# Kernel optimization log

Hardware: AMD Instinct MI355X
Metric: run time of the kernel (lower is better)

## Reference

```python
import jax, jax.numpy as jnp
import numpy as np

GF_R = 49      # guided filter radius (hardcoded in module)
GF_EPS = 1.0   # guided filter eps (hardcoded in module)


def edge_pad(x, r):
    # replicate-pad last two dims by r
    return jnp.pad(x, ((0, 0), (0, 0), (r, r), (r, r)), mode='edge')


def boxfilter(x, r):
    # integral-image box filter via cumsum chains, same shape out
    p = edge_pad(x, r)
    c = jnp.cumsum(p, axis=3)
    d = c[:, :, :, 2 * r:] - c[:, :, :, :-2 * r]
    c2 = jnp.cumsum(d, axis=2)
    return c2[:, :, 2 * r:, :] - c2[:, :, :-2 * r, :]


def guided_filter(x, r=GF_R, eps=GF_EPS):
    N = boxfilter(jnp.ones_like(x), r)
    mean_x = boxfilter(x, r) / N
    mean_x2 = boxfilter(x * x, r) / N
    var_x = mean_x2 - mean_x * mean_x   # cov_xy == var_x in the original code
    A = var_x / (var_x + eps)
    bb = mean_x - A * mean_x
    A = boxfilter(A, r) / N
    bb = boxfilter(bb, r) / N
    return A * x + bb


def setup_inputs() -> dict:
    key = jax.random.key(0)
    ks = jax.random.split(key, 12)
    m, n, r = 2048, 4096, 4
    m3 = len(np.arange(m)[::3])  # 683
    return {
        'b': jax.random.normal(ks[0], (1, 1, m, n), jnp.float32),
        'b_negative': jax.random.normal(ks[1], (1, 1, m3, n), jnp.float32),
        'foreground_b': jax.random.uniform(ks[2], (1, 1, m, n), jnp.float32),
        'hX': jax.random.normal(ks[3], (1, 1, m * r, n), jnp.float32),
        'recon_old': jax.random.normal(ks[4], (1, 1, m, n), jnp.float32),
        'fusion_mask': jax.random.uniform(ks[5], (1, 1, m, n), jnp.float32),
        'b_old': jax.random.normal(ks[6], (1, 1, m, n), jnp.float32),
        'r': r,
        'w': jax.random.normal(ks[7], (m, n), jnp.float32),
        'decay_col': jax.random.normal(ks[8], (1, 1, m3, n), jnp.float32),
        'ww': jax.random.normal(ks[9], (m, n), jnp.float32),
    }


def reference(b, b_negative, foreground_b, hX, recon_old, fusion_mask, b_old, r, w, decay_col, ww):
    m, n = w.shape
    b = b * jax.nn.softplus(w)
    # cumsum over coarse rows then bilinear upsample to (m, n)
    decay = jnp.cumsum(b_negative * jax.nn.softplus(decay_col), axis=-2)
    decay = jax.image.resize(decay, (1, 1, m, n), method='linear')
    b = jnp.cumsum(b, axis=-2)
    b = b + decay * (1.0 - foreground_b)
    b_adpt = b * fusion_mask + b_old * (1.0 - fusion_mask)
    diff = guided_filter(hX[:, :, ::r, :] + b_adpt - recon_old)
    diff_adpt = jnp.clip(jnp.diff(diff, axis=-2, prepend=diff[:, :, 0:1, :]), 0.0, None)
    diff_adpt = diff_adpt * jax.nn.softplus(ww)
    diff_adpt = jnp.cumsum(diff_adpt, axis=-2)
    b_adpt = b_adpt - diff_adpt
    return (b_adpt, diff, diff_adpt, b)
```

## Files before the change

kernel.cpp:

```cpp
#include <hip/hip_runtime.h>
#include <cstdint>
#include <cstddef>

#define MR 2048
#define NC 4096
#define M3 683
#define SEG 64
#define HSEG 32
#define SEGD 22
#define H3D 32
#define VT 64
#define VTILES 32
#define NORM (1.0f/9604.0f)

__device__ __forceinline__ float sp(float v){
  return fmaxf(v, 0.0f) + log1pf(expf(-fabsf(v)));
}


__global__ void seg_sum_decay(const float* __restrict__ bneg, const float* __restrict__ dcol,
                              float* __restrict__ TD, float* __restrict__ Pd){
  int s = blockIdx.x;
  int j = blockIdx.y*blockDim.x + threadIdx.x;
  int i0 = s*H3D, i1 = min(M3, i0+H3D);
  float acc = 0.f;
  for(int i=i0;i<i1;i++){
    float t = bneg[i*NC+j]*sp(dcol[i*NC+j]);
    TD[i*NC+j]=t;
    acc += t;
  }
  Pd[s*NC+j] = acc;
}

__global__ void seg_sum_b(const float* __restrict__ b, const float* __restrict__ w,
                          float* __restrict__ TB, float* __restrict__ Pb){
  int s = blockIdx.x;
  int j = blockIdx.y*blockDim.x + threadIdx.x;
  int i0 = s*HSEG;
  float acc=0.f;
  #pragma unroll 4
  for(int i=i0;i<i0+HSEG;i++){
    float t = b[i*NC+j]*sp(w[i*NC+j]);
    TB[i*NC+j]=t;
    acc += t;
  }
  Pb[s*NC+j]=acc;
}

__global__ void scan_excl(float* __restrict__ P, int segs){
  int j = blockIdx.x*blockDim.x + threadIdx.x;
  float run=0.f;
  for(int s=0;s<segs;s++){
    float t = P[s*NC+j];
    P[s*NC+j] = run;
    run += t;
  }
}

__global__ void decay_finalize(const float* __restrict__ TD,
                               const float* __restrict__ Pd, float* __restrict__ dc){
  int s=blockIdx.x;
  int j=blockIdx.y*blockDim.x+threadIdx.x;
  int i0=s*H3D, i1=min(M3,i0+H3D);
  float run = Pd[s*NC+j];
  for(int i=i0;i<i1;i++){
    run += TD[i*NC+j];
    dc[i*NC+j]=run;
  }
}

__global__ void phase1(const float* __restrict__ TB,
                       const float* __restrict__ Pb, const float* __restrict__ dc,
                       const float* __restrict__ fg, const float* __restrict__ fm,
                       const float* __restrict__ bold, const float* __restrict__ hX,
                       const float* __restrict__ recon,
                       float* __restrict__ out0, float* __restrict__ out3,
                       float* __restrict__ X){
  int s=blockIdx.x;
  int j=blockIdx.y*blockDim.x+threadIdx.x;
  int i0=s*HSEG;
  float run = Pb[s*NC+j];
  #pragma unroll 4
  for(int rr=0;rr<HSEG;rr++){
    int i=i0+rr;
    run += TB[i*NC+j];
    float c = (i+0.5f)*(683.0f/2048.0f)-0.5f;
    float fl = floorf(c);
    float f = c-fl;
    int a0=(int)fl, a1=a0+1;
    a0 = a0<0?0:(a0>M3-1?M3-1:a0);
    a1 = a1<0?0:(a1>M3-1?M3-1:a1);
    float d = (1.f-f)*dc[a0*NC+j] + f*dc[a1*NC+j];
    float bf = run + d*(1.f - fg[i*NC+j]);
    out3[i*NC+j]=bf;
    float fmv = fm[i*NC+j];
    float ba = bf*fmv + bold[i*NC+j]*(1.f-fmv);
    out0[i*NC+j]=ba;
    X[i*NC+j] = hX[(4*i)*NC+j] + ba - recon[i*NC+j];
  }
}


__global__ __launch_bounds__(256) void hbox_sq(const float* __restrict__ X,
                         float* __restrict__ H1, float* __restrict__ H2){
  __shared__ float C1[NC+1];
  __shared__ float C2[NC+1];
  __shared__ float ts1[256];
  __shared__ float ts2[256];
  int row=blockIdx.x, tid=threadIdx.x;
  const float* xr = X + (size_t)row*NC;
  float v1[16], v2[16];
  int base=tid*16;
  float run1=0.f,run2=0.f;
  const float4* p4 = reinterpret_cast<const float4*>(xr+base);
  #pragma unroll
  for(int q=0;q<4;q++){
    float4 fq=p4[q];
    float e[4]={fq.x,fq.y,fq.z,fq.w};
    #pragma unroll
    for(int t=0;t<4;t++){
      run1+=e[t];      v1[q*4+t]=run1;
      run2+=e[t]*e[t]; v2[q*4+t]=run2;
    }
  }
  ts1[tid]=run1; ts2[tid]=run2;
  __syncthreads();
  for(int off=1; off<256; off<<=1){
    float a1 = (tid>=off)? ts1[tid-off]:0.f;
    float a2 = (tid>=off)? ts2[tid-off]:0.f;
    __syncthreads();
    ts1[tid]+=a1; ts2[tid]+=a2;
    __syncthreads();
  }
  float ex1 = ts1[tid]-run1, ex2 = ts2[tid]-run2;
  if(tid==0){C1[0]=0.f;C2[0]=0.f;}
  #pragma unroll
  for(int e=0;e<16;e++){ C1[base+1+e]=ex1+v1[e]; C2[base+1+e]=ex2+v2[e]; }
  __syncthreads();
  float first1=C1[1],       last1=C1[NC]-C1[NC-1];
  float first2=C2[1],       last2=C2[NC]-C2[NC-1];
  float* h1 = H1+(size_t)row*NC;
  float* h2 = H2+(size_t)row*NC;
  #pragma unroll
  for(int k=0;k<16;k++){
    int j=k*256+tid;
    int lo=j-48, hi=j+49;
    int li = lo<0?0:lo;
    int hc = hi>NC-1?NC-1:hi;
    float s1=C1[hc+1]-C1[li];
    float s2=C2[hc+1]-C2[li];
    if(lo<0){ s1+=(float)(-lo)*first1; s2+=(float)(-lo)*first2; }
    if(hi>NC-1){ s1+=(float)(hi-(NC-1))*last1; s2+=(float)(hi-(NC-1))*last2; }
    h1[j]=s1; h2[j]=s2;
  }
}

__global__ __launch_bounds__(256) void hbox_two(const float* __restrict__ A,
                         const float* __restrict__ B,
                         float* __restrict__ H1, float* __restrict__ H2){
  __shared__ float C1[NC+1];
  __shared__ float C2[NC+1];
  __shared__ float ts1[256];
  __shared__ float ts2[256];
  int row=blockIdx.x, tid=threadIdx.x;
  const float* ar = A + (size_t)row*NC;
  const float* br = B + (size_t)row*NC;
  float v1[16], v2[16];
  int base=tid*16;
  float run1=0.f,run2=0.f;
  const float4* pa = reinterpret_cast<const float4*>(ar+base);
  const float4* pb = reinterpret_cast<const float4*>(br+base);
  #pragma unroll
  for(int q=0;q<4;q++){
    float4 fa=pa[q]; float4 fb=pb[q];
    float ea[4]={fa.x,fa.y,fa.z,fa.w};
    float eb[4]={fb.x,fb.y,fb.z,fb.w};
    #pragma unroll
    for(int t=0;t<4;t++){
      run1+=ea[t]; v1[q*4+t]=run1;
      run2+=eb[t]; v2[q*4+t]=run2;
    }
  }
  ts1[tid]=run1; ts2[tid]=run2;
  __syncthreads();
  for(int off=1; off<256; off<<=1){
    float a1 = (tid>=off)? ts1[tid-off]:0.f;
    float a2 = (tid>=off)? ts2[tid-off]:0.f;
    __syncthreads();
    ts1[tid]+=a1; ts2[tid]+=a2;
    __syncthreads();
  }
  float ex1 = ts1[tid]-run1, ex2 = ts2[tid]-run2;
  if(tid==0){C1[0]=0.f;C2[0]=0.f;}
  #pragma unroll
  for(int e=0;e<16;e++){ C1[base+1+e]=ex1+v1[e]; C2[base+1+e]=ex2+v2[e]; }
  __syncthreads();
  float first1=C1[1], last1=C1[NC]-C1[NC-1];
  float first2=C2[1], last2=C2[NC]-C2[NC-1];
  float* h1 = H1+(size_t)row*NC;
  float* h2 = H2+(size_t)row*NC;
  #pragma unroll
  for(int k=0;k<16;k++){
    int j=k*256+tid;
    int lo=j-48, hi=j+49;
    int li = lo<0?0:lo;
    int hc = hi>NC-1?NC-1:hi;
    float s1=C1[hc+1]-C1[li];
    float s2=C2[hc+1]-C2[li];
    if(lo<0){ s1+=(float)(-lo)*first1; s2+=(float)(-lo)*first2; }
    if(hi>NC-1){ s1+=(float)(hi-(NC-1))*last1; s2+=(float)(hi-(NC-1))*last2; }
    h1[j]=s1; h2[j]=s2;
  }
}


__global__ void vbox_stage1(const float* __restrict__ H1, const float* __restrict__ H2,
                            float* __restrict__ Aimg, float* __restrict__ BBimg){
  int tile = blockIdx.x;
  int j = blockIdx.y*blockDim.x + threadIdx.x;
  int i0 = tile*VT;
  float Sa=0.f, Sb=0.f;
  for(int c=i0-48;c<=i0+49;c++){
    int cc = c<0?0:(c>MR-1?MR-1:c);
    Sa += H1[cc*NC+j]; Sb += H2[cc*NC+j];
  }
  #pragma unroll 4
  for(int rr=0;rr<VT;rr++){
    int i=i0+rr;
    if(rr>0){
      int up = i+49; up = up>MR-1?MR-1:up;
      int dn = i-49; dn = dn<0?0:dn;
      Sa += H1[up*NC+j]-H1[dn*NC+j];
      Sb += H2[up*NC+j]-H2[dn*NC+j];
    }
    float mx = Sa*NORM, mx2 = Sb*NORM;
    float var = mx2 - mx*mx;
    float A = var/(var+1.0f);
    float bb = mx - A*mx;
    Aimg[i*NC+j]=A; BBimg[i*NC+j]=bb;
  }
}


__global__ void vbox2_fused(const float* __restrict__ H1, const float* __restrict__ H2,
                            const float* __restrict__ X, const float* __restrict__ ww,
                            float* __restrict__ diff, float* __restrict__ S,
                            float* __restrict__ Pc){
  int tile = blockIdx.x;
  int j = blockIdx.y*blockDim.x + threadIdx.x;
  int i0 = tile*VT;
  int istart = (tile==0)? 0 : i0-1;
  float Sa=0.f, Sb=0.f;
  for(int c=istart-48;c<=istart+49;c++){
    int cc = c<0?0:(c>MR-1?MR-1:c);
    Sa += H1[cc*NC+j]; Sb += H2[cc*NC+j];
  }
  float dpre, acc=0.f;
  if(tile==0){
    float d0 = (Sa*NORM)*X[j] + Sb*NORM;
    diff[j]=d0; S[j]=0.f; dpre=d0;
    for(int i=1;i<VT;i++){
      int up = i+49; up = up>MR-1?MR-1:up;
      int dn = i-49; dn = dn<0?0:dn;
      Sa += H1[up*NC+j]-H1[dn*NC+j];
      Sb += H2[up*NC+j]-H2[dn*NC+j];
      float d = (Sa*NORM)*X[i*NC+j] + Sb*NORM;
      diff[i*NC+j]=d;
      float v = d-dpre; v = v>0.f? v:0.f;
      float sv = v*sp(ww[i*NC+j]);
      S[i*NC+j]=sv; acc+=sv; dpre=d;
    }
  } else {
    dpre = (Sa*NORM)*X[(size_t)istart*NC+j] + Sb*NORM;
    for(int rr=0;rr<VT;rr++){
      int i=i0+rr;
      int up = i+49; up = up>MR-1?MR-1:up;
      int dn = i-49; dn = dn<0?0:dn;
      Sa += H1[up*NC+j]-H1[dn*NC+j];
      Sb += H2[up*NC+j]-H2[dn*NC+j];
      float d = (Sa*NORM)*X[i*NC+j] + Sb*NORM;
      diff[i*NC+j]=d;
      float v = d-dpre; v = v>0.f? v:0.f;
      float sv = v*sp(ww[i*NC+j]);
      S[i*NC+j]=sv; acc+=sv; dpre=d;
    }
  }
  Pc[tile*NC+j]=acc;
}


__global__ void phase3_final(const float* __restrict__ Pc,
                             float* __restrict__ out0, float* __restrict__ out2){
  int s=blockIdx.x;
  int j=blockIdx.y*blockDim.x+threadIdx.x;
  int i0=s*VT;
  float run = Pc[s*NC+j];
  #pragma unroll 4
  for(int rr=0;rr<VT;rr++){
    int i=i0+rr;
    run += out2[i*NC+j];
    out2[i*NC+j]=run;
    out0[i*NC+j]=out0[i*NC+j]-run;
  }
}

extern "C" void kernel_launch(void* const* d_in, const int* in_sizes, int n_in,
                              void* d_out, int out_size, void* d_ws, size_t ws_size,
                              hipStream_t stream){
  const float* b    = (const float*)d_in[0];
  const float* bneg = (const float*)d_in[1];
  const float* fg   = (const float*)d_in[2];
  const float* hX   = (const float*)d_in[3];
  const float* recon= (const float*)d_in[4];
  const float* fm   = (const float*)d_in[5];
  const float* bold = (const float*)d_in[6];
  const float* w    = (const float*)d_in[8];
  const float* dcol = (const float*)d_in[9];
  const float* ww   = (const float*)d_in[10];

  float* out  = (float*)d_out;
  float* out0 = out;
  float* out1 = out + (size_t)MR*NC;
  float* out2 = out + 2ull*MR*NC;
  float* out3 = out + 3ull*MR*NC;

  float* wsf = (float*)d_ws;
  float* X  = wsf;
  float* H1 = wsf + 1ull*MR*NC;
  float* H2 = wsf + 2ull*MR*NC;
  float* DC = wsf + 3ull*MR*NC;
  float* Pb = DC + (size_t)M3*NC;
  float* Pd = Pb + (size_t)SEG*NC;
  float* Pc = Pd + (size_t)SEGD*NC;
  float* TD = H1;
  float* TB = H2;

  seg_sum_decay<<<dim3(SEGD,NC/256),256,0,stream>>>(bneg,dcol,TD,Pd);
  seg_sum_b    <<<dim3(SEG, NC/256),256,0,stream>>>(b,w,TB,Pb);
  scan_excl    <<<NC/256,256,0,stream>>>(Pd,SEGD);
  scan_excl    <<<NC/256,256,0,stream>>>(Pb,SEG);
  decay_finalize<<<dim3(SEGD,NC/256),256,0,stream>>>(TD,Pd,DC);
  phase1       <<<dim3(SEG, NC/256),256,0,stream>>>(TB,Pb,DC,fg,fm,bold,hX,recon,out0,out3,X);
  hbox_sq      <<<MR,256,0,stream>>>(X,H1,H2);
  vbox_stage1  <<<dim3(VTILES,NC/256),256,0,stream>>>(H1,H2,out1,out2);
  hbox_two     <<<MR,256,0,stream>>>(out1,out2,H1,H2);
  vbox2_fused  <<<dim3(VTILES,NC/256),256,0,stream>>>(H1,H2,X,ww,out1,out2,Pc);
  scan_excl    <<<NC/256,256,0,stream>>>(Pc,VTILES);
  phase3_final <<<dim3(VTILES,NC/256),256,0,stream>>>(Pc,out0,out2);
}
```

Before: 696.7 us.

## Batch loads for memory parallelism, wave-shuffle scans, padded LDS in box filters

Column-wise streaming kernels (segment sums, scans, decay finalize, vertical box passes, final scan) now load 8–14 rows into registers before computing, so more global loads are in flight per thread. The horizontal box kernels replace the shared-memory Hillis-Steele scan with a wave-level shuffle scan plus a small cross-wave combine, dropping many barriers. They also pad the LDS prefix arrays to reduce bank conflicts. The vertical pass is rewritten to start every tile one row early, which handles tile 0 with a large sentinel instead of a special branch. The cost is higher register pressure and therefore possibly lower occupancy.

```diff
diff --git a/kernel.cpp b/kernel.cpp
--- a/kernel.cpp
+++ b/kernel.cpp
@@ -12,6 +12,7 @@
 #define VT 64
 #define VTILES 32
 #define NORM (1.0f/9604.0f)
+#define SK(k) ((k)+((k)>>4))
 
 __device__ __forceinline__ float sp(float v){
   return fmaxf(v, 0.0f) + log1pf(expf(-fabsf(v)));
@@ -24,11 +25,15 @@
   int j = blockIdx.y*blockDim.x + threadIdx.x;
   int i0 = s*H3D, i1 = min(M3, i0+H3D);
   float acc = 0.f;
-  for(int i=i0;i<i1;i++){
-    float t = bneg[i*NC+j]*sp(dcol[i*NC+j]);
-    TD[i*NC+j]=t;
-    acc += t;
-  }
+  int i = i0;
+  for(; i+8<=i1; i+=8){
+    float bv[8], dv[8];
+    #pragma unroll
+    for(int t=0;t<8;t++){ bv[t]=bneg[(i+t)*NC+j]; dv[t]=dcol[(i+t)*NC+j]; }
+    #pragma unroll
+    for(int t=0;t<8;t++){ float x=bv[t]*sp(dv[t]); TD[(i+t)*NC+j]=x; acc+=x; }
+  }
+  for(; i<i1; i++){ float x=bneg[i*NC+j]*sp(dcol[i*NC+j]); TD[i*NC+j]=x; acc+=x; }
   Pd[s*NC+j] = acc;
 }
 
@@ -38,23 +43,29 @@
   int j = blockIdx.y*blockDim.x + threadIdx.x;
   int i0 = s*HSEG;
   float acc=0.f;
-  #pragma unroll 4
-  for(int i=i0;i<i0+HSEG;i++){
-    float t = b[i*NC+j]*sp(w[i*NC+j]);
-    TB[i*NC+j]=t;
-    acc += t;
+  for(int g=0;g<HSEG;g+=8){
+    float bv[8], wv[8];
+    #pragma unroll
+    for(int t=0;t<8;t++){ int i=i0+g+t; bv[t]=b[i*NC+j]; wv[t]=w[i*NC+j]; }
+    #pragma unroll
+    for(int t=0;t<8;t++){ int i=i0+g+t; float x=bv[t]*sp(wv[t]); TB[i*NC+j]=x; acc+=x; }
   }
   Pb[s*NC+j]=acc;
 }
 
-__global__ void scan_excl(float* __restrict__ P, int segs){
+template<int SEGS>
+__global__ void scan_excl_t(float* __restrict__ P){
   int j = blockIdx.x*blockDim.x + threadIdx.x;
   float run=0.f;
-  for(int s=0;s<segs;s++){
-    float t = P[s*NC+j];
-    P[s*NC+j] = run;
-    run += t;
-  }
+  int s=0;
+  for(; s+8<=SEGS; s+=8){
+    float v[8];
+    #pragma unroll
+    for(int t=0;t<8;t++) v[t]=P[(s+t)*NC+j];
+    #pragma unroll
+    for(int t=0;t<8;t++){ P[(s+t)*NC+j]=run; run+=v[t]; }
+  }
+  for(; s<SEGS; s++){ float t=P[s*NC+j]; P[s*NC+j]=run; run+=t; }
 }
 
 __global__ void decay_finalize(const float* __restrict__ TD,
@@ -63,10 +74,15 @@
   int j=blockIdx.y*blockDim.x+threadIdx.x;
   int i0=s*H3D, i1=min(M3,i0+H3D);
   float run = Pd[s*NC+j];
-  for(int i=i0;i<i1;i++){
-    run += TD[i*NC+j];
-    dc[i*NC+j]=run;
-  }
+  int i=i0;
+  for(; i+8<=i1; i+=8){
+    float tv[8];
+    #pragma unroll
+    for(int t=0;t<8;t++) tv[t]=TD[(i+t)*NC+j];
+    #pragma unroll
+    for(int t=0;t<8;t++){ run+=tv[t]; dc[(i+t)*NC+j]=run; }
+  }
+  for(; i<i1; i++){ run += TD[i*NC+j]; dc[i*NC+j]=run; }
 }
 
 __global__ void phase1(const float* __restrict__ TB,
@@ -103,11 +119,12 @@
 
 __global__ __launch_bounds__(256) void hbox_sq(const float* __restrict__ X,
                          float* __restrict__ H1, float* __restrict__ H2){
-  __shared__ float C1[NC+1];
-  __shared__ float C2[NC+1];
-  __shared__ float ts1[256];
-  __shared__ float ts2[256];
+  __shared__ float C1[SK(NC)+1];
+  __shared__ float C2[SK(NC)+1];
+  __shared__ float w1[4];
+  __shared__ float w2[4];
   int row=blockIdx.x, tid=threadIdx.x;
+  int lane = tid & 63, wvid = tid >> 6;
   const float* xr = X + (size_t)row*NC;
   float v1[16], v2[16];
   int base=tid*16;
@@ -123,22 +140,25 @@
       run2+=e[t]*e[t]; v2[q*4+t]=run2;
     }
   }
-  ts1[tid]=run1; ts2[tid]=run2;
+  float s1=run1, s2=run2;
+  #pragma unroll
+  for(int off=1;off<64;off<<=1){
+    float o1=__shfl_up(s1,off);
+    float o2=__shfl_up(s2,off);
+    if(lane>=off){ s1+=o1; s2+=o2; }
+  }
+  if(lane==63){ w1[wvid]=s1; w2[wvid]=s2; }
   __syncthreads();
-  for(int off=1; off<256; off<<=1){
-    float a1 = (tid>=off)? ts1[tid-off]:0.f;
-    float a2 = (tid>=off)? ts2[tid-off]:0.f;
-    __syncthreads();
-    ts1[tid]+=a1; ts2[tid]+=a2;
-    __syncthreads();
-  }
-  float ex1 = ts1[tid]-run1, ex2 = ts2[tid]-run2;
-  if(tid==0){C1[0]=0.f;C2[0]=0.f;}
-  #pragma unroll
-  for(int e=0;e<16;e++){ C1[base+1+e]=ex1+v1[e]; C2[base+1+e]=ex2+v2[e]; }
+  float b1=0.f,b2=0.f;
+  #pragma unroll
+  for(int q=0;q<4;q++) if(q<wvid){ b1+=w1[q]; b2+=w2[q]; }
+  float ex1 = b1 + s1 - run1, ex2 = b2 + s2 - run2;
+  if(tid==0){C1[SK(0)]=0.f;C2[SK(0)]=0.f;}
+  #pragma unroll
+  for(int e=0;e<16;e++){ int k=base+1+e; C1[SK(k)]=ex1+v1[e]; C2[SK(k)]=ex2+v2[e]; }
   __syncthreads();
-  float first1=C1[1],       last1=C1[NC]-C1[NC-1];
-  float first2=C2[1],       last2=C2[NC]-C2[NC-1];
+  float first1=C1[SK(1)],  last1=C1[SK(NC)]-C1[SK(NC-1)];
+  float first2=C2[SK(1)],  last2=C2[SK(NC)]-C2[SK(NC-1)];
   float* h1 = H1+(size_t)row*NC;
   float* h2 = H2+(size_t)row*NC;
   #pragma unroll
@@ -147,22 +167,23 @@
     int lo=j-48, hi=j+49;
     int li = lo<0?0:lo;
     int hc = hi>NC-1?NC-1:hi;
-    float s1=C1[hc+1]-C1[li];
-    float s2=C2[hc+1]-C2[li];
-    if(lo<0){ s1+=(float)(-lo)*first1; s2+=(float)(-lo)*first2; }
-    if(hi>NC-1){ s1+=(float)(hi-(NC-1))*last1; s2+=(float)(hi-(NC-1))*last2; }
-    h1[j]=s1; h2[j]=s2;
+    float s1w=C1[SK(hc+1)]-C1[SK(li)];
+    float s2w=C2[SK(hc+1)]-C2[SK(li)];
+    if(lo<0){ s1w+=(float)(-lo)*first1; s2w+=(float)(-lo)*first2; }
+    if(hi>NC-1){ s1w+=(float)(hi-(NC-1))*last1; s2w+=(float)(hi-(NC-1))*last2; }
+    h1[j]=s1w; h2[j]=s2w;
   }
 }
 
 __global__ __launch_bounds__(256) void hbox_two(const float* __restrict__ A,
                          const float* __restrict__ B,
                          float* __restrict__ H1, float* __restrict__ H2){
-  __shared__ float C1[NC+1];
-  __shared__ float C2[NC+1];
-  __shared__ float ts1[256];
-  __shared__ float ts2[256];
+  __shared__ float C1[SK(NC)+1];
+  __shared__ float C2[SK(NC)+1];
+  __shared__ float w1[4];
+  __shared__ float w2[4];
   int row=blockIdx.x, tid=threadIdx.x;
+  int lane = tid & 63, wvid = tid >> 6;
   const float* ar = A + (size_t)row*NC;
   const float* br = B + (size_t)row*NC;
   float v1[16], v2[16];
@@ -181,22 +202,25 @@
       run2+=eb[t]; v2[q*4+t]=run2;
     }
   }
-  ts1[tid]=run1; ts2[tid]=run2;
+  float s1=run1, s2=run2;
+  #pragma unroll
+  for(int off=1;off<64;off<<=1){
+    float o1=__shfl_up(s1,off);
+    float o2=__shfl_up(s2,off);
+    if(lane>=off){ s1+=o1; s2+=o2; }
+  }
+  if(lane==63){ w1[wvid]=s1; w2[wvid]=s2; }
   __syncthreads();
-  for(int off=1; off<256; off<<=1){
-    float a1 = (tid>=off)? ts1[tid-off]:0.f;
-    float a2 = (tid>=off)? ts2[tid-off]:0.f;
-    __syncthreads();
-    ts1[tid]+=a1; ts2[tid]+=a2;
-    __syncthreads();
-  }
-  float ex1 = ts1[tid]-run1, ex2 = ts2[tid]-run2;
-  if(tid==0){C1[0]=0.f;C2[0]=0.f;}
-  #pragma unroll
-  for(int e=0;e<16;e++){ C1[base+1+e]=ex1+v1[e]; C2[base+1+e]=ex2+v2[e]; }
+  float b1=0.f,b2=0.f;
+  #pragma unroll
+  for(int q=0;q<4;q++) if(q<wvid){ b1+=w1[q]; b2+=w2[q]; }
+  float ex1 = b1 + s1 - run1, ex2 = b2 + s2 - run2;
+  if(tid==0){C1[SK(0)]=0.f;C2[SK(0)]=0.f;}
+  #pragma unroll
+  for(int e=0;e<16;e++){ int k=base+1+e; C1[SK(k)]=ex1+v1[e]; C2[SK(k)]=ex2+v2[e]; }
   __syncthreads();
-  float first1=C1[1], last1=C1[NC]-C1[NC-1];
-  float first2=C2[1], last2=C2[NC]-C2[NC-1];
+  float first1=C1[SK(1)], last1=C1[SK(NC)]-C1[SK(NC-1)];
+  float first2=C2[SK(1)], last2=C2[SK(NC)]-C2[SK(NC-1)];
   float* h1 = H1+(size_t)row*NC;
   float* h2 = H2+(size_t)row*NC;
   #pragma unroll
@@ -205,11 +229,11 @@
     int lo=j-48, hi=j+49;
     int li = lo<0?0:lo;
     int hc = hi>NC-1?NC-1:hi;
-    float s1=C1[hc+1]-C1[li];
-    float s2=C2[hc+1]-C2[li];
-    if(lo<0){ s1+=(float)(-lo)*first1; s2+=(float)(-lo)*first2; }
-    if(hi>NC-1){ s1+=(float)(hi-(NC-1))*last1; s2+=(float)(hi-(NC-1))*last2; }
-    h1[j]=s1; h2[j]=s2;
+    float s1w=C1[SK(hc+1)]-C1[SK(li)];
+    float s2w=C2[SK(hc+1)]-C2[SK(li)];
+    if(lo<0){ s1w+=(float)(-lo)*first1; s2w+=(float)(-lo)*first2; }
+    if(hi>NC-1){ s1w+=(float)(hi-(NC-1))*last1; s2w+=(float)(hi-(NC-1))*last2; }
+    h1[j]=s1w; h2[j]=s2w;
   }
 }
 
@@ -219,25 +243,40 @@
   int tile = blockIdx.x;
   int j = blockIdx.y*blockDim.x + threadIdx.x;
   int i0 = tile*VT;
+  int ip = i0-1;
   float Sa=0.f, Sb=0.f;
-  for(int c=i0-48;c<=i0+49;c++){
-    int cc = c<0?0:(c>MR-1?MR-1:c);
-    Sa += H1[cc*NC+j]; Sb += H2[cc*NC+j];
-  }
-  #pragma unroll 4
-  for(int rr=0;rr<VT;rr++){
-    int i=i0+rr;
-    if(rr>0){
-      int up = i+49; up = up>MR-1?MR-1:up;
-      int dn = i-49; dn = dn<0?0:dn;
-      Sa += H1[up*NC+j]-H1[dn*NC+j];
-      Sb += H2[up*NC+j]-H2[dn*NC+j];
-    }
-    float mx = Sa*NORM, mx2 = Sb*NORM;
-    float var = mx2 - mx*mx;
-    float A = var/(var+1.0f);
-    float bb = mx - A*mx;
-    Aimg[i*NC+j]=A; BBimg[i*NC+j]=bb;
+  for(int g=0; g<98; g+=14){
+    float a1[14], a2[14];
+    #pragma unroll
+    for(int t=0;t<14;t++){
+      int c = ip-48+g+t;
+      int cc = c<0?0:(c>MR-1?MR-1:c);
+      a1[t]=H1[cc*NC+j]; a2[t]=H2[cc*NC+j];
+    }
+    #pragma unroll
+    for(int t=0;t<14;t++){ Sa+=a1[t]; Sb+=a2[t]; }
+  }
+  for(int g=0; g<VT; g+=8){
+    float hu1[8],hd1[8],hu2[8],hd2[8];
+    #pragma unroll
+    for(int t=0;t<8;t++){
+      int i=i0+g+t;
+      int up=i+49; up=up>MR-1?MR-1:up;
+      int dn=i-49; dn=dn<0?0:dn;
+      hu1[t]=H1[up*NC+j]; hd1[t]=H1[dn*NC+j];
+      hu2[t]=H2[up*NC+j]; hd2[t]=H2[dn*NC+j];
+    }
+    #pragma unroll
+    for(int t=0;t<8;t++){
+      int i=i0+g+t;
+      Sa += hu1[t]-hd1[t];
+      Sb += hu2[t]-hd2[t];
+      float mx = Sa*NORM, mx2 = Sb*NORM;
+      float var = mx2 - mx*mx;
+      float A = var/(var+1.0f);
+      float bb = mx - A*mx;
+      Aimg[i*NC+j]=A; BBimg[i*NC+j]=bb;
+    }
   }
 }
 
@@ -249,39 +288,42 @@
   int tile = blockIdx.x;
   int j = blockIdx.y*blockDim.x + threadIdx.x;
   int i0 = tile*VT;
-  int istart = (tile==0)? 0 : i0-1;
+  int ip = i0-1;
   float Sa=0.f, Sb=0.f;
-  for(int c=istart-48;c<=istart+49;c++){
-    int cc = c<0?0:(c>MR-1?MR-1:c);
-    Sa += H1[cc*NC+j]; Sb += H2[cc*NC+j];
+  for(int g=0; g<98; g+=14){
+    float a1[14], a2[14];
+    #pragma unroll
+    for(int t=0;t<14;t++){
+      int c = ip-48+g+t;
+      int cc = c<0?0:(c>MR-1?MR-1:c);
+      a1[t]=H1[cc*NC+j]; a2[t]=H2[cc*NC+j];
+    }
+    #pragma unroll
+    for(int t=0;t<14;t++){ Sa+=a1[t]; Sb+=a2[t]; }
   }
   float dpre, acc=0.f;
-  if(tile==0){
-    float d0 = (Sa*NORM)*X[j] + Sb*NORM;
-    diff[j]=d0; S[j]=0.f; dpre=d0;
-    for(int i=1;i<VT;i++){
-      int up = i+49; up = up>MR-1?MR-1:up;
-      int dn = i-49; dn = dn<0?0:dn;
-      Sa += H1[up*NC+j]-H1[dn*NC+j];
-      Sb += H2[up*NC+j]-H2[dn*NC+j];
-      float d = (Sa*NORM)*X[i*NC+j] + Sb*NORM;
+  if(tile==0) dpre = 3.0e38f;
+  else        dpre = (Sa*NORM)*X[(size_t)ip*NC+j] + Sb*NORM;
+  for(int g=0; g<VT; g+=8){
+    float hu1[8],hd1[8],hu2[8],hd2[8],xv[8],wv[8];
+    #pragma unroll
+    for(int t=0;t<8;t++){
+      int i=i0+g+t;
+      int up=i+49; up=up>MR-1?MR-1:up;
+      int dn=i-49; dn=dn<0?0:dn;
+      hu1[t]=H1[up*NC+j]; hd1[t]=H1[dn*NC+j];
+      hu2[t]=H2[up*NC+j]; hd2[t]=H2[dn*NC+j];
+      xv[t]=X[(size_t)i*NC+j]; wv[t]=ww[i*NC+j];
+    }
+    #pragma unroll
+    for(int t=0;t<8;t++){
+      int i=i0+g+t;
+      Sa += hu1[t]-hd1[t];
+      Sb += hu2[t]-hd2[t];
+      float d = (Sa*NORM)*xv[t] + Sb*NORM;
       diff[i*NC+j]=d;
       float v = d-dpre; v = v>0.f? v:0.f;
-      float sv = v*sp(ww[i*NC+j]);
-      S[i*NC+j]=sv; acc+=sv; dpre=d;
-    }
-  } else {
-    dpre = (Sa*NORM)*X[(size_t)istart*NC+j] + Sb*NORM;
-    for(int rr=0;rr<VT;rr++){
-      int i=i0+rr;
-      int up = i+49; up = up>MR-1?MR-1:up;
-      int dn = i-49; dn = dn<0?0:dn;
-      Sa += H1[up*NC+j]-H1[dn*NC+j];
-      Sb += H2[up*NC+j]-H2[dn*NC+j];
-      float d = (Sa*NORM)*X[i*NC+j] + Sb*NORM;
-      diff[i*NC+j]=d;
-      float v = d-dpre; v = v>0.f? v:0.f;
-      float sv = v*sp(ww[i*NC+j]);
+      float sv = v*sp(wv[t]);
       S[i*NC+j]=sv; acc+=sv; dpre=d;
     }
   }
@@ -295,12 +337,17 @@
   int j=blockIdx.y*blockDim.x+threadIdx.x;
   int i0=s*VT;
   float run = Pc[s*NC+j];
-  #pragma unroll 4
-  for(int rr=0;rr<VT;rr++){
-    int i=i0+rr;
-    run += out2[i*NC+j];
-    out2[i*NC+j]=run;
-    out0[i*NC+j]=out0[i*NC+j]-run;
+  for(int g=0; g<VT; g+=8){
+    float sv[8], o0[8];
+    #pragma unroll
+    for(int t=0;t<8;t++){ int i=i0+g+t; sv[t]=out2[i*NC+j]; o0[t]=out0[i*NC+j]; }
+    #pragma unroll
+    for(int t=0;t<8;t++){
+      int i=i0+g+t;
+      run += sv[t];
+      out2[i*NC+j]=run;
+      out0[i*NC+j]=o0[t]-run;
+    }
   }
 }
 
@@ -337,14 +384,14 @@
 
   seg_sum_decay<<<dim3(SEGD,NC/256),256,0,stream>>>(bneg,dcol,TD,Pd);
   seg_sum_b    <<<dim3(SEG, NC/256),256,0,stream>>>(b,w,TB,Pb);
-  scan_excl    <<<NC/256,256,0,stream>>>(Pd,SEGD);
-  scan_excl    <<<NC/256,256,0,stream>>>(Pb,SEG);
+  scan_excl_t<SEGD><<<NC/256,256,0,stream>>>(Pd);
+  scan_excl_t<SEG> <<<NC/256,256,0,stream>>>(Pb);
   decay_finalize<<<dim3(SEGD,NC/256),256,0,stream>>>(TD,Pd,DC);
   phase1       <<<dim3(SEG, NC/256),256,0,stream>>>(TB,Pb,DC,fg,fm,bold,hX,recon,out0,out3,X);
   hbox_sq      <<<MR,256,0,stream>>>(X,H1,H2);
   vbox_stage1  <<<dim3(VTILES,NC/256),256,0,stream>>>(H1,H2,out1,out2);
   hbox_two     <<<MR,256,0,stream>>>(out1,out2,H1,H2);
   vbox2_fused  <<<dim3(VTILES,NC/256),256,0,stream>>>(H1,H2,X,ww,out1,out2,Pc);
-  scan_excl    <<<NC/256,256,0,stream>>>(Pc,VTILES);
+  scan_excl_t<VTILES><<<NC/256,256,0,stream>>>(Pc);
   phase3_final <<<dim3(VTILES,NC/256),256,0,stream>>>(Pc,out0,out2);
 }
```

New measurement: 569.3 us. -18.3%, faster.
